# Optimization experiments

Measured on AMD Instinct MI355X. Metric: run time of the kernel, lower is better.

Reference implementation:

```python
import jax, jax.numpy as jnp
import numpy as np

DIM = 1024
HEADS = 16
DIM_HEAD = 64
INNER = HEADS * DIM_HEAD
SEQ = 4096
BATCH = 1


def setup_inputs() -> dict:
    key = jax.random.key(0)
    ks = jax.random.split(key, 6)
    s = 0.02
    return {
        "x": jax.random.normal(ks[0], (BATCH, SEQ, DIM), dtype=jnp.float32),
        "Wq": jax.random.normal(ks[1], (DIM, INNER), dtype=jnp.float32) * s,
        "Wk": jax.random.normal(ks[2], (DIM, INNER), dtype=jnp.float32) * s,
        "Wv": jax.random.normal(ks[3], (DIM, INNER), dtype=jnp.float32) * s,
        "Wo": jax.random.normal(ks[4], (INNER, DIM), dtype=jnp.float32) * s,
        "bo": jax.random.normal(ks[5], (DIM,), dtype=jnp.float32) * s,
    }


def reference(x, Wq, Wk, Wv, Wo, bo):
    b, n, _ = x.shape
    beta = 1.0 / jnp.sqrt(jnp.float32(DIM_HEAD))
    # project and split heads: [b, n, inner] -> [b, h, n, d]
    def split_heads(t):
        return t.reshape(b, n, HEADS, DIM_HEAD).transpose(0, 2, 1, 3)
    q = split_heads(x @ Wq)
    k = split_heads(x @ Wk)
    v = split_heads(x @ Wv)
    # scaled scores [b, h, n, n]
    scores = jnp.einsum('bhid,bhjd->bhij', q * beta, k)
    mask_value = -jnp.finfo(scores.dtype).max
    causal = jnp.triu(jnp.ones((n, n), dtype=bool), k=1)
    scores = jnp.where(causal, mask_value, scores)
    attn = jax.nn.softmax(scores, axis=-1)
    out = jnp.einsum('bhij,bhjd->bhid', attn, v)
    out = out.transpose(0, 2, 1, 3).reshape(b, n, INNER)
    # output projection (dropout is identity in eval)
    return out @ Wo + bo
```

## Files before the change

kernel.cpp:

```cpp
#include <hip/hip_runtime.h>
#include <hip/hip_bf16.h>
#include <stdint.h>
#include <math.h>

#define SEQ 4096
#define DIM 1024
#define NHEADS 16
#define DHEAD 64
#define INNER 1024

typedef __hip_bfloat16 bf16;
typedef __attribute__((ext_vector_type(8))) short short8;
typedef __attribute__((ext_vector_type(4))) float floatx4;

__device__ __forceinline__ void gll16(const bf16* g, bf16* l) {
    __builtin_amdgcn_global_load_lds(
        (const __attribute__((address_space(1))) unsigned int*)g,
        (__attribute__((address_space(3))) unsigned int*)l,
        16, 0, 0);
}

__device__ __forceinline__ unsigned short f2bf_bits(float f) {
    bf16 h = __float2bfloat16(f);
    return *reinterpret_cast<unsigned short*>(&h);
}

__device__ __forceinline__ uint2 pack4bf(float a, float b, float c, float d) {
    __hip_bfloat162 lo = __float22bfloat162_rn(float2{a, b});
    __hip_bfloat162 hi = __float22bfloat162_rn(float2{c, d});
    uint2 r;
    r.x = *reinterpret_cast<unsigned*>(&lo);
    r.y = *reinterpret_cast<unsigned*>(&hi);
    return r;
}

__global__ __launch_bounds__(256) void prep_kernel(
        const float* __restrict__ x, const float* __restrict__ W0,
        const float* __restrict__ W1, const float* __restrict__ W2,
        const float* __restrict__ W3, bf16* __restrict__ xb,
        bf16* __restrict__ T0, bf16* __restrict__ T1,
        bf16* __restrict__ T2, bf16* __restrict__ T3) {
    const int tid = threadIdx.x + threadIdx.y * blockDim.x;
    if (blockIdx.z == 4) {
        int chunk = blockIdx.y * 32 + blockIdx.x;
        int base = chunk * 4096 + tid * 4;
        #pragma unroll
        for (int r = 0; r < 4; r++) {
            int i = base + r * 1024;
            float4 f = *reinterpret_cast<const float4*>(x + i);
            unsigned long long p = (unsigned long long)f2bf_bits(f.x)
                                 | ((unsigned long long)f2bf_bits(f.y) << 16)
                                 | ((unsigned long long)f2bf_bits(f.z) << 32)
                                 | ((unsigned long long)f2bf_bits(f.w) << 48);
            *reinterpret_cast<unsigned long long*>(xb + i) = p;
        }
        return;
    }
    const float* W; bf16* T;
    switch (blockIdx.z) {
        case 0:  W = W0; T = T0; break;
        case 1:  W = W1; T = T1; break;
        case 2:  W = W2; T = T2; break;
        default: W = W3; T = T3; break;
    }
    __shared__ float tile[32][33];
    int k0 = blockIdx.x * 32, n0 = blockIdx.y * 32;
    int tx = threadIdx.x, ty = threadIdx.y;
    #pragma unroll
    for (int i = 0; i < 4; i++)
        tile[ty + 8 * i][tx] = W[(size_t)(k0 + ty + 8 * i) * 1024 + n0 + tx];
    __syncthreads();
    #pragma unroll
    for (int i = 0; i < 4; i++)
        T[(size_t)(n0 + ty + 8 * i) * 1024 + k0 + tx] = __float2bfloat16(tile[tx][ty + 8 * i]);
}

__device__ __forceinline__ void gemm128_body(const bf16* __restrict__ A,
                                             const bf16* __restrict__ Bt,
                                             int m0, int n0, floatx4 acc[4][4]) {
    __shared__ __align__(16) bf16 As[8192];
    __shared__ __align__(16) bf16 Bs[8192];
    const int tid = threadIdx.x;
    const int wave = tid >> 6;
    const int lane = tid & 63;
    const int l15 = lane & 15;
    const int quad = lane >> 4;

    #pragma unroll
    for (int i = 0; i < 4; i++)
        #pragma unroll
        for (int j = 0; j < 4; j++)
            acc[i][j] = (floatx4){0.f, 0.f, 0.f, 0.f};

    for (int k0 = 0; k0 < 1024; k0 += 64) {
        __syncthreads();
        #pragma unroll
        for (int j = 0; j < 4; j++) {
            int t = wave * 4 + j;
            int row = (t >> 1) * 16 + l15;
            int kb = (t & 1) * 32 + quad * 8;
            gll16(A + (size_t)(m0 + row) * 1024 + k0 + kb, &As[t * 512]);
            gll16(Bt + (size_t)(n0 + row) * 1024 + k0 + kb, &Bs[t * 512]);
        }
        __syncthreads();
        #pragma unroll
        for (int ks = 0; ks < 2; ks++) {
            short8 af[4], bfr[4];
            #pragma unroll
            for (int i = 0; i < 4; i++)
                af[i] = *reinterpret_cast<const short8*>(
                    &As[((((wave >> 1) * 4 + i) * 2 + ks) * 512) + lane * 8]);
            #pragma unroll
            for (int j = 0; j < 4; j++)
                bfr[j] = *reinterpret_cast<const short8*>(
                    &Bs[((((wave & 1) * 4 + j) * 2 + ks) * 512) + lane * 8]);
            #pragma unroll
            for (int i = 0; i < 4; i++)
                #pragma unroll
                for (int j = 0; j < 4; j++)
                    acc[i][j] = __builtin_amdgcn_mfma_f32_16x16x32_bf16(af[i], bfr[j], acc[i][j], 0, 0, 0);
        }
    }
}

__global__ __launch_bounds__(256) void qkv_gemm_kernel(
        const bf16* __restrict__ xb,
        const bf16* __restrict__ Wqt, const bf16* __restrict__ Wkt, const bf16* __restrict__ Wvt,
        bf16* __restrict__ Qh, bf16* __restrict__ Kh, bf16* __restrict__ Vt) {
    const bf16* Bt;
    if (blockIdx.z == 0)      Bt = Wqt;
    else if (blockIdx.z == 1) Bt = Wkt;
    else                      Bt = Wvt;
    int n0 = blockIdx.x * 128, m0 = blockIdx.y * 128;
    floatx4 acc[4][4];
    gemm128_body(xb, Bt, m0, n0, acc);

    const int tid = threadIdx.x, wave = tid >> 6, lane = tid & 63;
    const int l15 = lane & 15, quad = lane >> 4;
    const int wm = (wave >> 1) * 64, wn = (wave & 1) * 64;
    if (blockIdx.z == 2) {
        #pragma unroll
        for (int i = 0; i < 4; i++)
            #pragma unroll
            for (int j = 0; j < 4; j++) {
                int col = n0 + wn + j * 16 + l15;
                int h = col >> 6, d = col & 63;
                int row0 = m0 + wm + i * 16 + quad * 4;
                uint2 v = pack4bf(acc[i][j][0], acc[i][j][1], acc[i][j][2], acc[i][j][3]);
                *reinterpret_cast<uint2*>(Vt + ((size_t)h * DHEAD + d) * SEQ + row0) = v;
            }
    } else {
        bf16* O = (blockIdx.z == 0) ? Qh : Kh;
        float scale = (blockIdx.z == 0) ? 0.125f * 1.4426950408889634f : 1.0f;
        #pragma unroll
        for (int i = 0; i < 4; i++)
            #pragma unroll
            for (int j = 0; j < 4; j++) {
                int col = n0 + wn + j * 16 + l15;
                int h = col >> 6, d = col & 63;
                #pragma unroll
                for (int r = 0; r < 4; r++) {
                    int row = m0 + wm + i * 16 + quad * 4 + r;
                    O[((size_t)h * SEQ + row) * DHEAD + d] = __float2bfloat16(acc[i][j][r] * scale);
                }
            }
    }
}

__global__ __launch_bounds__(256) void out_gemm_kernel(
        const bf16* __restrict__ Oa, const bf16* __restrict__ Wot,
        const float* __restrict__ bo, float* __restrict__ out) {
    int n0 = blockIdx.x * 128, m0 = blockIdx.y * 128;
    floatx4 acc[4][4];
    gemm128_body(Oa, Wot, m0, n0, acc);

    const int tid = threadIdx.x, wave = tid >> 6, lane = tid & 63;
    const int l15 = lane & 15, quad = lane >> 4;
    const int wm = (wave >> 1) * 64, wn = (wave & 1) * 64;
    #pragma unroll
    for (int i = 0; i < 4; i++)
        #pragma unroll
        for (int j = 0; j < 4; j++) {
            int col = n0 + wn + j * 16 + l15;
            float b = bo[col];
            #pragma unroll
            for (int r = 0; r < 4; r++) {
                int row = m0 + wm + i * 16 + quad * 4 + r;
                out[(size_t)row * DIM + col] = acc[i][j][r] + b;
            }
        }
}

__global__ __launch_bounds__(256, 4) void attention_kernel(
        const bf16* __restrict__ Qh, const bf16* __restrict__ Kh,
        const bf16* __restrict__ Vt, bf16* __restrict__ Oa) {
    __shared__ __align__(16) bf16 Ksh[2][4096];
    __shared__ __align__(16) bf16 Vsh[2][4096];
    __shared__ __align__(16) bf16 Ps[4][1024];
    const int tid = threadIdx.x, wave = tid >> 6, lane = tid & 63;
    const int l15 = lane & 15, quad = lane >> 4;
    const int id = blockIdx.x;
    const int head = id & 15;
    const int rk = id >> 4;
    const int r0 = rk & 15, bsel = (rk >> 4) & 1, c2 = rk >> 5;
    const int qt = bsel ? (2 * r0 + c2) : (63 - 2 * r0 - c2);
    const int qw = qt * 64 + wave * 16;
    const size_t hoff = (size_t)head * SEQ * DHEAD;
    const bf16* Qb = Qh + hoff;
    const bf16* Kb = Kh + hoff;
    const bf16* Vb = Vt + hoff;

    short8 bq[2];
    #pragma unroll
    for (int s = 0; s < 2; s++)
        bq[s] = *reinterpret_cast<const short8*>(
            Qb + (size_t)(qw + l15) * DHEAD + s * 32 + quad * 8);

    floatx4 acc_o[4];
    #pragma unroll
    for (int c = 0; c < 4; c++) acc_o[c] = (floatx4){0.f, 0.f, 0.f, 0.f};
    float l_part = 0.f;

    auto stage = [&](int buf, int kbase) {
        #pragma unroll
        for (int j = 0; j < 2; j++) {
            int t = wave * 2 + j;
            gll16(Kb + (size_t)(kbase + (t >> 1) * 16 + l15) * DHEAD + (t & 1) * 32 + quad * 8,
                  &Ksh[buf][t * 512]);
            gll16(Vb + (size_t)((t >> 1) * 16 + l15) * SEQ + kbase + (t & 1) * 32 + quad * 8,
                  &Vsh[buf][t * 512]);
        }
    };

    const int ntiles = qt + 1;
    stage(0, 0);
    __syncthreads();
    int cur = 0;
    for (int kt = 0; kt < ntiles; kt++) {
        const int kbase = kt * 64;
        if (kt + 1 < ntiles) stage(cur ^ 1, (kt + 1) * 64);

        floatx4 st[4];
        #pragma unroll
        for (int c = 0; c < 4; c++) st[c] = (floatx4){0.f, 0.f, 0.f, 0.f};
        __builtin_amdgcn_s_setprio(1);
        #pragma unroll
        for (int c = 0; c < 4; c++) {
            short8 ak0 = *reinterpret_cast<const short8*>(&Ksh[cur][(c * 2 + 0) * 512 + lane * 8]);
            short8 ak1 = *reinterpret_cast<const short8*>(&Ksh[cur][(c * 2 + 1) * 512 + lane * 8]);
            st[c] = __builtin_amdgcn_mfma_f32_16x16x32_bf16(ak0, bq[0], st[c], 0, 0, 0);
            st[c] = __builtin_amdgcn_mfma_f32_16x16x32_bf16(ak1, bq[1], st[c], 0, 0, 0);
        }
        __builtin_amdgcn_s_setprio(0);
        if (kbase + 63 > qw) {
            int base0 = kbase + quad * 4 - qw - l15;
            #pragma unroll
            for (int c = 0; c < 4; c++) {
                int base = base0 + c * 16;
                #pragma unroll
                for (int r = 0; r < 4; r++)
                    if (base + r > 0) st[c][r] = -1e30f;
            }
        }
        #pragma unroll
        for (int c = 0; c < 4; c++) {
            float p0 = __builtin_amdgcn_exp2f(st[c][0]);
            float p1 = __builtin_amdgcn_exp2f(st[c][1]);
            float p2 = __builtin_amdgcn_exp2f(st[c][2]);
            float p3 = __builtin_amdgcn_exp2f(st[c][3]);
            l_part += (p0 + p1) + (p2 + p3);
            int elem = (c >> 1) * 512
                     + (l15 + 16 * ((c & 1) * 2 + (quad >> 1))) * 8 + (quad & 1) * 4;
            *reinterpret_cast<uint2*>(&Ps[wave][elem]) = pack4bf(p0, p1, p2, p3);
        }
        __builtin_amdgcn_s_setprio(1);
        #pragma unroll
        for (int s = 0; s < 2; s++) {
            short8 bp = *reinterpret_cast<const short8*>(&Ps[wave][s * 512 + lane * 8]);
            #pragma unroll
            for (int c = 0; c < 4; c++) {
                short8 av = *reinterpret_cast<const short8*>(&Vsh[cur][(c * 2 + s) * 512 + lane * 8]);
                acc_o[c] = __builtin_amdgcn_mfma_f32_16x16x32_bf16(av, bp, acc_o[c], 0, 0, 0);
            }
        }
        __builtin_amdgcn_s_setprio(0);

        __syncthreads();
        cur ^= 1;
    }
    float l = l_part;
    l += __shfl_xor(l, 16, 64);
    l += __shfl_xor(l, 32, 64);
    float rcp = 1.0f / l;
    const int q = qw + l15;
    #pragma unroll
    for (int c = 0; c < 4; c++) {
        uint2 v = pack4bf(acc_o[c][0] * rcp, acc_o[c][1] * rcp,
                          acc_o[c][2] * rcp, acc_o[c][3] * rcp);
        *reinterpret_cast<uint2*>(Oa + (size_t)q * INNER + head * DHEAD + c * 16 + quad * 4) = v;
    }
}

extern "C" void kernel_launch(void* const* d_in, const int* in_sizes, int n_in,
                              void* d_out, int out_size, void* d_ws, size_t ws_size,
                              hipStream_t stream) {
    const float* x  = (const float*)d_in[0];
    const float* Wq = (const float*)d_in[1];
    const float* Wk = (const float*)d_in[2];
    const float* Wv = (const float*)d_in[3];
    const float* Wo = (const float*)d_in[4];
    const float* bo = (const float*)d_in[5];
    float* out = (float*)d_out;

    char* ws = (char*)d_ws;
    size_t off = 0;
    bf16* xb  = (bf16*)(ws + off); off += (size_t)SEQ * DIM * 2;
    bf16* Wqt = (bf16*)(ws + off); off += (size_t)DIM * INNER * 2;
    bf16* Wkt = (bf16*)(ws + off); off += (size_t)DIM * INNER * 2;
    bf16* Wvt = (bf16*)(ws + off); off += (size_t)DIM * INNER * 2;
    bf16* Wot = (bf16*)(ws + off); off += (size_t)INNER * DIM * 2;
    bf16* Qh  = (bf16*)(ws + off); off += (size_t)NHEADS * SEQ * DHEAD * 2;
    bf16* Kh  = (bf16*)(ws + off); off += (size_t)NHEADS * SEQ * DHEAD * 2;
    bf16* Vtr = (bf16*)(ws + off); off += (size_t)NHEADS * DHEAD * SEQ * 2;
    bf16* Oa  = (bf16*)(ws + off); off += (size_t)SEQ * INNER * 2;

    prep_kernel<<<dim3(32, 32, 5), dim3(32, 8), 0, stream>>>(x, Wq, Wk, Wv, Wo,
                                                             xb, Wqt, Wkt, Wvt, Wot);
    qkv_gemm_kernel<<<dim3(8, 32, 3), 256, 0, stream>>>(xb, Wqt, Wkt, Wvt, Qh, Kh, Vtr);
    attention_kernel<<<1024, 256, 0, stream>>>(Qh, Kh, Vtr, Oa);
    out_gemm_kernel<<<dim3(8, 32), 256, 0, stream>>>(Oa, Wot, bo, out);
}
```

Before: 260.5 us.

## Process 128 query rows per attention block to reuse K/V tiles

Each wave now handles two 16-row query groups (32 rows), so a block covers 128 queries and every staged K/V tile in shared memory feeds twice as many MFMAs. The grid is halved to 512 blocks and the causal load-balancing map is changed to pair tile i with tile 31-i. The goal is to halve K/V global loads and LDS traffic per unit of compute. The cost is more registers (launch bounds lowered to 2), a larger P buffer in shared memory, fewer blocks, and wasted masked work on the diagonal tiles.

```diff
diff --git a/kernel.cpp b/kernel.cpp
--- a/kernel.cpp
+++ b/kernel.cpp
@@ -191,35 +191,39 @@
         }
 }
 
-__global__ __launch_bounds__(256, 4) void attention_kernel(
+__global__ __launch_bounds__(256, 2) void attention_kernel(
         const bf16* __restrict__ Qh, const bf16* __restrict__ Kh,
         const bf16* __restrict__ Vt, bf16* __restrict__ Oa) {
     __shared__ __align__(16) bf16 Ksh[2][4096];
     __shared__ __align__(16) bf16 Vsh[2][4096];
-    __shared__ __align__(16) bf16 Ps[4][1024];
+    __shared__ __align__(16) bf16 Ps[4][2048];
     const int tid = threadIdx.x, wave = tid >> 6, lane = tid & 63;
     const int l15 = lane & 15, quad = lane >> 4;
     const int id = blockIdx.x;
     const int head = id & 15;
     const int rk = id >> 4;
-    const int r0 = rk & 15, bsel = (rk >> 4) & 1, c2 = rk >> 5;
-    const int qt = bsel ? (2 * r0 + c2) : (63 - 2 * r0 - c2);
-    const int qw = qt * 64 + wave * 16;
+    const int qtile = (rk < 16) ? rk : 47 - rk;
+    const int qbase = qtile * 128;
+    const int qw = qbase + wave * 32;
     const size_t hoff = (size_t)head * SEQ * DHEAD;
     const bf16* Qb = Qh + hoff;
     const bf16* Kb = Kh + hoff;
     const bf16* Vb = Vt + hoff;
 
-    short8 bq[2];
-    #pragma unroll
-    for (int s = 0; s < 2; s++)
-        bq[s] = *reinterpret_cast<const short8*>(
-            Qb + (size_t)(qw + l15) * DHEAD + s * 32 + quad * 8);
-
-    floatx4 acc_o[4];
-    #pragma unroll
-    for (int c = 0; c < 4; c++) acc_o[c] = (floatx4){0.f, 0.f, 0.f, 0.f};
-    float l_part = 0.f;
+    short8 bq[2][2];
+    #pragma unroll
+    for (int g = 0; g < 2; g++)
+        #pragma unroll
+        for (int s = 0; s < 2; s++)
+            bq[g][s] = *reinterpret_cast<const short8*>(
+                Qb + (size_t)(qw + g * 16 + l15) * DHEAD + s * 32 + quad * 8);
+
+    floatx4 acc_o[2][4];
+    #pragma unroll
+    for (int g = 0; g < 2; g++)
+        #pragma unroll
+        for (int c = 0; c < 4; c++) acc_o[g][c] = (floatx4){0.f, 0.f, 0.f, 0.f};
+    float l_part[2] = {0.f, 0.f};
 
     auto stage = [&](int buf, int kbase) {
         #pragma unroll
@@ -232,7 +236,7 @@
         }
     };
 
-    const int ntiles = qt + 1;
+    const int ntiles = 2 * qtile + 2;
     stage(0, 0);
     __syncthreads();
     int cur = 0;
@@ -240,47 +244,58 @@
         const int kbase = kt * 64;
         if (kt + 1 < ntiles) stage(cur ^ 1, (kt + 1) * 64);
 
-        floatx4 st[4];
-        #pragma unroll
-        for (int c = 0; c < 4; c++) st[c] = (floatx4){0.f, 0.f, 0.f, 0.f};
+        floatx4 st[2][4];
+        #pragma unroll
+        for (int g = 0; g < 2; g++)
+            #pragma unroll
+            for (int c = 0; c < 4; c++) st[g][c] = (floatx4){0.f, 0.f, 0.f, 0.f};
         __builtin_amdgcn_s_setprio(1);
         #pragma unroll
         for (int c = 0; c < 4; c++) {
             short8 ak0 = *reinterpret_cast<const short8*>(&Ksh[cur][(c * 2 + 0) * 512 + lane * 8]);
             short8 ak1 = *reinterpret_cast<const short8*>(&Ksh[cur][(c * 2 + 1) * 512 + lane * 8]);
-            st[c] = __builtin_amdgcn_mfma_f32_16x16x32_bf16(ak0, bq[0], st[c], 0, 0, 0);
-            st[c] = __builtin_amdgcn_mfma_f32_16x16x32_bf16(ak1, bq[1], st[c], 0, 0, 0);
+            st[0][c] = __builtin_amdgcn_mfma_f32_16x16x32_bf16(ak0, bq[0][0], st[0][c], 0, 0, 0);
+            st[0][c] = __builtin_amdgcn_mfma_f32_16x16x32_bf16(ak1, bq[0][1], st[0][c], 0, 0, 0);
+            st[1][c] = __builtin_amdgcn_mfma_f32_16x16x32_bf16(ak0, bq[1][0], st[1][c], 0, 0, 0);
+            st[1][c] = __builtin_amdgcn_mfma_f32_16x16x32_bf16(ak1, bq[1][1], st[1][c], 0, 0, 0);
         }
         __builtin_amdgcn_s_setprio(0);
-        if (kbase + 63 > qw) {
-            int base0 = kbase + quad * 4 - qw - l15;
+        #pragma unroll
+        for (int g = 0; g < 2; g++) {
+            if (kbase + 63 > qw + g * 16) {
+                int base0 = kbase + quad * 4 - (qw + g * 16) - l15;
+                #pragma unroll
+                for (int c = 0; c < 4; c++) {
+                    int base = base0 + c * 16;
+                    #pragma unroll
+                    for (int r = 0; r < 4; r++)
+                        if (base + r > 0) st[g][c][r] = -1e30f;
+                }
+            }
+        }
+        #pragma unroll
+        for (int g = 0; g < 2; g++)
             #pragma unroll
             for (int c = 0; c < 4; c++) {
-                int base = base0 + c * 16;
-                #pragma unroll
-                for (int r = 0; r < 4; r++)
-                    if (base + r > 0) st[c][r] = -1e30f;
-            }
-        }
-        #pragma unroll
-        for (int c = 0; c < 4; c++) {
-            float p0 = __builtin_amdgcn_exp2f(st[c][0]);
-            float p1 = __builtin_amdgcn_exp2f(st[c][1]);
-            float p2 = __builtin_amdgcn_exp2f(st[c][2]);
-            float p3 = __builtin_amdgcn_exp2f(st[c][3]);
-            l_part += (p0 + p1) + (p2 + p3);
-            int elem = (c >> 1) * 512
-                     + (l15 + 16 * ((c & 1) * 2 + (quad >> 1))) * 8 + (quad & 1) * 4;
-            *reinterpret_cast<uint2*>(&Ps[wave][elem]) = pack4bf(p0, p1, p2, p3);
-        }
+                float p0 = __builtin_amdgcn_exp2f(st[g][c][0]);
+                float p1 = __builtin_amdgcn_exp2f(st[g][c][1]);
+                float p2 = __builtin_amdgcn_exp2f(st[g][c][2]);
+                float p3 = __builtin_amdgcn_exp2f(st[g][c][3]);
+                l_part[g] += (p0 + p1) + (p2 + p3);
+                int elem = ((c >> 1) * 2 + g) * 512
+                         + (l15 + 16 * ((c & 1) * 2 + (quad >> 1))) * 8 + (quad & 1) * 4;
+                *reinterpret_cast<uint2*>(&Ps[wave][elem]) = pack4bf(p0, p1, p2, p3);
+            }
         __builtin_amdgcn_s_setprio(1);
         #pragma unroll
         for (int s = 0; s < 2; s++) {
-            short8 bp = *reinterpret_cast<const short8*>(&Ps[wave][s * 512 + lane * 8]);
+            short8 bp0 = *reinterpret_cast<const short8*>(&Ps[wave][(s * 2 + 0) * 512 + lane * 8]);
+            short8 bp1 = *reinterpret_cast<const short8*>(&Ps[wave][(s * 2 + 1) * 512 + lane * 8]);
             #pragma unroll
             for (int c = 0; c < 4; c++) {
                 short8 av = *reinterpret_cast<const short8*>(&Vsh[cur][(c * 2 + s) * 512 + lane * 8]);
-                acc_o[c] = __builtin_amdgcn_mfma_f32_16x16x32_bf16(av, bp, acc_o[c], 0, 0, 0);
+                acc_o[0][c] = __builtin_amdgcn_mfma_f32_16x16x32_bf16(av, bp0, acc_o[0][c], 0, 0, 0);
+                acc_o[1][c] = __builtin_amdgcn_mfma_f32_16x16x32_bf16(av, bp1, acc_o[1][c], 0, 0, 0);
             }
         }
         __builtin_amdgcn_s_setprio(0);
@@ -288,16 +303,19 @@
         __syncthreads();
         cur ^= 1;
     }
-    float l = l_part;
-    l += __shfl_xor(l, 16, 64);
-    l += __shfl_xor(l, 32, 64);
-    float rcp = 1.0f / l;
-    const int q = qw + l15;
-    #pragma unroll
-    for (int c = 0; c < 4; c++) {
-        uint2 v = pack4bf(acc_o[c][0] * rcp, acc_o[c][1] * rcp,
-                          acc_o[c][2] * rcp, acc_o[c][3] * rcp);
-        *reinterpret_cast<uint2*>(Oa + (size_t)q * INNER + head * DHEAD + c * 16 + quad * 4) = v;
+    #pragma unroll
+    for (int g = 0; g < 2; g++) {
+        float l = l_part[g];
+        l += __shfl_xor(l, 16, 64);
+        l += __shfl_xor(l, 32, 64);
+        float rcp = 1.0f / l;
+        const int q = qw + g * 16 + l15;
+        #pragma unroll
+        for (int c = 0; c < 4; c++) {
+            uint2 v = pack4bf(acc_o[g][c][0] * rcp, acc_o[g][c][1] * rcp,
+                              acc_o[g][c][2] * rcp, acc_o[g][c][3] * rcp);
+            *reinterpret_cast<uint2*>(Oa + (size_t)q * INNER + head * DHEAD + c * 16 + quad * 4) = v;
+        }
     }
 }
 
@@ -327,6 +345,6 @@
     prep_kernel<<<dim3(32, 32, 5), dim3(32, 8), 0, stream>>>(x, Wq, Wk, Wv, Wo,
                                                              xb, Wqt, Wkt, Wvt, Wot);
     qkv_gemm_kernel<<<dim3(8, 32, 3), 256, 0, stream>>>(xb, Wqt, Wkt, Wvt, Qh, Kh, Vtr);
-    attention_kernel<<<1024, 256, 0, stream>>>(Qh, Kh, Vtr, Oa);
+    attention_kernel<<<512, 256, 0, stream>>>(Qh, Kh, Vtr, Oa);
     out_gemm_kernel<<<dim3(8, 32), 256, 0, stream>>>(Oa, Wot, bo, out);
 }
```

New measurement: 275.3 us. 5.7% more time.

## Split long causal attention rows across two KV chunks with a combine pass

Applied to the files above, without the earlier changes.

Query tiles in the second half of the sequence are split into two work items, each covering half the key range, so the longest blocks become shorter and load balance across CUs improves. Partial unnormalized outputs and row sums go to fp32 workspace buffers. A new combine kernel sums the two partials and normalizes before writing bf16 output. This adds an extra launch and fp32 traffic, and it relies on a shared fixed softmax max offset, since no running max is combined.

```diff
diff --git a/kernel.cpp b/kernel.cpp
--- a/kernel.cpp
+++ b/kernel.cpp
@@ -193,7 +193,9 @@
 
 __global__ __launch_bounds__(256, 4) void attention_kernel(
         const bf16* __restrict__ Qh, const bf16* __restrict__ Kh,
-        const bf16* __restrict__ Vt, bf16* __restrict__ Oa) {
+        const bf16* __restrict__ Vt, bf16* __restrict__ Oa,
+        float* __restrict__ Op0, float* __restrict__ Op1,
+        float* __restrict__ L0, float* __restrict__ L1) {
     __shared__ __align__(16) bf16 Ksh[2][4096];
     __shared__ __align__(16) bf16 Vsh[2][4096];
     __shared__ __align__(16) bf16 Ps[4][1024];
@@ -202,8 +204,15 @@
     const int id = blockIdx.x;
     const int head = id & 15;
     const int rk = id >> 4;
-    const int r0 = rk & 15, bsel = (rk >> 4) & 1, c2 = rk >> 5;
-    const int qt = bsel ? (2 * r0 + c2) : (63 - 2 * r0 - c2);
+    int qt, ck;
+    if (rk < 32) { qt = 32 + rk; ck = 0; }
+    else {
+        int j = rk - 32, pair = j >> 1;
+        if ((j & 1) == 0) { qt = 63 - pair; ck = 1; }
+        else              { qt = 31 - pair; ck = 0; }
+    }
+    const int ktile0 = ck ? 32 : 0;
+    const int ktile1 = (qt < 32) ? (qt + 1) : (ck ? (qt + 1) : 32);
     const int qw = qt * 64 + wave * 16;
     const size_t hoff = (size_t)head * SEQ * DHEAD;
     const bf16* Qb = Qh + hoff;
@@ -232,13 +241,12 @@
         }
     };
 
-    const int ntiles = qt + 1;
-    stage(0, 0);
+    stage(0, ktile0 * 64);
     __syncthreads();
     int cur = 0;
-    for (int kt = 0; kt < ntiles; kt++) {
+    for (int kt = ktile0; kt < ktile1; kt++) {
         const int kbase = kt * 64;
-        if (kt + 1 < ntiles) stage(cur ^ 1, (kt + 1) * 64);
+        if (kt + 1 < ktile1) stage(cur ^ 1, (kt + 1) * 64);
 
         floatx4 st[4];
         #pragma unroll
@@ -291,14 +299,41 @@
     float l = l_part;
     l += __shfl_xor(l, 16, 64);
     l += __shfl_xor(l, 32, 64);
+    const int q = qw + l15;
+    if (qt < 32) {
+        float rcp = 1.0f / l;
+        #pragma unroll
+        for (int c = 0; c < 4; c++) {
+            uint2 v = pack4bf(acc_o[c][0] * rcp, acc_o[c][1] * rcp,
+                              acc_o[c][2] * rcp, acc_o[c][3] * rcp);
+            *reinterpret_cast<uint2*>(Oa + (size_t)q * INNER + head * DHEAD + c * 16 + quad * 4) = v;
+        }
+    } else {
+        float* Op = ck ? Op1 : Op0;
+        float* Lp = ck ? L1 : L0;
+        if (quad == 0) Lp[head * 2048 + (q - 2048)] = l;
+        #pragma unroll
+        for (int c = 0; c < 4; c++)
+            *reinterpret_cast<floatx4*>(
+                Op + (size_t)(q - 2048) * INNER + head * DHEAD + c * 16 + quad * 4) = acc_o[c];
+    }
+}
+
+__global__ __launch_bounds__(256) void combine_kernel(
+        const float* __restrict__ Op0, const float* __restrict__ Op1,
+        const float* __restrict__ L0, const float* __restrict__ L1,
+        bf16* __restrict__ Oa) {
+    int idx = blockIdx.x * 256 + threadIdx.x;
+    int row = idx >> 8;
+    int c4 = (idx & 255) * 4;
+    int head = c4 >> 6;
+    float l = L0[head * 2048 + row] + L1[head * 2048 + row];
     float rcp = 1.0f / l;
-    const int q = qw + l15;
-    #pragma unroll
-    for (int c = 0; c < 4; c++) {
-        uint2 v = pack4bf(acc_o[c][0] * rcp, acc_o[c][1] * rcp,
-                          acc_o[c][2] * rcp, acc_o[c][3] * rcp);
-        *reinterpret_cast<uint2*>(Oa + (size_t)q * INNER + head * DHEAD + c * 16 + quad * 4) = v;
-    }
+    float4 a = *reinterpret_cast<const float4*>(Op0 + (size_t)row * INNER + c4);
+    float4 b = *reinterpret_cast<const float4*>(Op1 + (size_t)row * INNER + c4);
+    uint2 v = pack4bf((a.x + b.x) * rcp, (a.y + b.y) * rcp,
+                      (a.z + b.z) * rcp, (a.w + b.w) * rcp);
+    *reinterpret_cast<uint2*>(Oa + (size_t)(2048 + row) * INNER + c4) = v;
 }
 
 extern "C" void kernel_launch(void* const* d_in, const int* in_sizes, int n_in,
@@ -323,10 +358,15 @@
     bf16* Kh  = (bf16*)(ws + off); off += (size_t)NHEADS * SEQ * DHEAD * 2;
     bf16* Vtr = (bf16*)(ws + off); off += (size_t)NHEADS * DHEAD * SEQ * 2;
     bf16* Oa  = (bf16*)(ws + off); off += (size_t)SEQ * INNER * 2;
+    float* Op0 = (float*)(ws + off); off += (size_t)(SEQ / 2) * INNER * 4;
+    float* Op1 = (float*)(ws + off); off += (size_t)(SEQ / 2) * INNER * 4;
+    float* L0  = (float*)(ws + off); off += (size_t)NHEADS * (SEQ / 2) * 4;
+    float* L1  = (float*)(ws + off); off += (size_t)NHEADS * (SEQ / 2) * 4;
 
     prep_kernel<<<dim3(32, 32, 5), dim3(32, 8), 0, stream>>>(x, Wq, Wk, Wv, Wo,
                                                              xb, Wqt, Wkt, Wvt, Wot);
     qkv_gemm_kernel<<<dim3(8, 32, 3), 256, 0, stream>>>(xb, Wqt, Wkt, Wvt, Qh, Kh, Vtr);
-    attention_kernel<<<1024, 256, 0, stream>>>(Qh, Kh, Vtr, Oa);
+    attention_kernel<<<1536, 256, 0, stream>>>(Qh, Kh, Vtr, Oa, Op0, Op1, L0, L1);
+    combine_kernel<<<2048, 256, 0, stream>>>(Op0, Op1, L0, L1, Oa);
     out_gemm_kernel<<<dim3(8, 32), 256, 0, stream>>>(Oa, Wot, bo, out);
 }
```

New measurement: 249.9 us. 1.04x faster.
